# Kernel tuning notes

Hardware: AMD Instinct MI355X
Metric: run time of the kernel (lower is better)

Reference implementation:

```python
import jax, jax.numpy as jnp
import numpy as np

D_MODEL = 1024
N_HEADS = 16
D_K = 64
CHUNK_LEN = 64
B, CHUNKS, NEIGHBORS, NEIGHBOR_LEN = 8, 32, 2, 128
SEQ = CHUNKS * CHUNK_LEN  # 2048
LN_EPS = 1e-5


def setup_inputs() -> dict:
    key = jax.random.key(0)
    ks = jax.random.split(key, 8)
    s = 0.02
    return {
        "h": jax.random.normal(ks[0], (B, SEQ, D_MODEL), dtype=jnp.float32),
        "e": jax.random.normal(ks[1], (B, CHUNKS, NEIGHBORS, NEIGHBOR_LEN, D_MODEL), dtype=jnp.float32),
        "Wq": jax.random.normal(ks[2], (D_MODEL, N_HEADS * D_K), dtype=jnp.float32) * s,
        "bq": jnp.zeros((N_HEADS * D_K,), dtype=jnp.float32),
        "Wk": jax.random.normal(ks[3], (D_MODEL, N_HEADS * D_K), dtype=jnp.float32) * s,
        "bk": jnp.zeros((N_HEADS * D_K,), dtype=jnp.float32),
        "Wv": jax.random.normal(ks[4], (D_MODEL, N_HEADS * D_K), dtype=jnp.float32) * s,
        "bv": jnp.zeros((N_HEADS * D_K,), dtype=jnp.float32),
        "gamma": jnp.ones((D_MODEL,), dtype=jnp.float32),
        "beta": jnp.zeros((D_MODEL,), dtype=jnp.float32),
        "Wo": jax.random.normal(ks[5], (N_HEADS * D_K, D_MODEL), dtype=jnp.float32) * s,
        "bo": jnp.zeros((D_MODEL,), dtype=jnp.float32),
    }


def _layer_norm(x, gamma, beta):
    mu = jnp.mean(x, axis=-1, keepdims=True)
    var = jnp.mean(jnp.square(x - mu), axis=-1, keepdims=True)
    return (x - mu) * jax.lax.rsqrt(var + LN_EPS) * gamma + beta


def reference(h, e, Wq, bq, Wk, bk, Wv, bv, gamma, beta, Wo, bo):
    batch, chunks, neighbors, neighbor_len, d_model = e.shape
    seq = h.shape[1]
    scale = 1.0 / np.sqrt(D_K)
    h_res = h

    # shift so each chunk attends only to completed retrieval chunks
    x = h[:, CHUNK_LEN - 1:]                      # [b, seq-(cl-1), d]
    x = _layer_norm(x, gamma, beta)
    pad = chunks * CHUNK_LEN - x.shape[1]
    x = jnp.pad(x, ((0, 0), (0, pad), (0, 0)))    # [b, chunks*cl, d]
    x = x.reshape(batch, chunks, CHUNK_LEN, d_model)

    q = (x @ Wq + bq).reshape(batch, chunks, CHUNK_LEN, N_HEADS, D_K)
    k = (e @ Wk + bk).reshape(batch, chunks, neighbors, neighbor_len, N_HEADS, D_K)
    v = (e @ Wv + bv).reshape(batch, chunks, neighbors, neighbor_len, N_HEADS, D_K)

    attn = jnp.einsum('bcihd,bcnjhd->bchinj', q, k) * scale   # [b,c,h,i,n,j]
    a_shape = attn.shape
    attn = jax.nn.softmax(attn.reshape(*a_shape[:4], -1), axis=-1).reshape(a_shape)

    o = jnp.einsum('bchinj,bcnjhd->bcihd', attn, v)           # [b,c,i,h,d]
    o = o.reshape(batch, chunks * CHUNK_LEN, N_HEADS * D_K)
    o = o @ Wo + bo
    # undo the shift: left-pad by chunk_len-1, truncate to seq
    o = jnp.pad(o, ((0, 0), (CHUNK_LEN - 1, 0), (0, 0)))[:, :seq]
    return o + h_res
```

## Files before the change

kernel.cpp:

```cpp
#include <hip/hip_runtime.h>
#include <hip/hip_bf16.h>

typedef __attribute__((ext_vector_type(8))) short bf16x8;
typedef __attribute__((ext_vector_type(4))) float f32x4;
typedef __attribute__((ext_vector_type(8))) unsigned short u16x8;

static __device__ __forceinline__ unsigned short f2bf(float f) {
  unsigned int u = __builtin_bit_cast(unsigned int, f);
  u += 0x7fffu + ((u >> 16) & 1u);
  return (unsigned short)(u >> 16);
}
static __device__ __forceinline__ unsigned int pk2(float lo, float hi) {
  return (unsigned int)f2bf(lo) | ((unsigned int)f2bf(hi) << 16);
}
static __device__ __forceinline__ void gload_lds16(const void* g, void* l) {
  __builtin_amdgcn_global_load_lds(
      (__attribute__((address_space(1))) void*)(g),
      (__attribute__((address_space(3))) void*)(l), 16, 0, 0);
}

__global__ __launch_bounds__(256) void cvt_bf16(const float* __restrict__ in,
                                                unsigned short* __restrict__ out,
                                                long n8) {
  const long stride = (long)gridDim.x * 256;
  for (long i = (long)blockIdx.x * 256 + threadIdx.x; i < n8; i += stride) {
    const float4 a = ((const float4*)in)[2 * i];
    const float4 b = ((const float4*)in)[2 * i + 1];
    uint4 w;
    w.x = pk2(a.x, a.y);
    w.y = pk2(a.z, a.w);
    w.z = pk2(b.x, b.y);
    w.w = pk2(b.z, b.w);
    ((uint4*)out)[i] = w;
  }
}

__global__ __launch_bounds__(256) void transpose_all(
    const float* __restrict__ Wq, const float* __restrict__ Wk,
    const float* __restrict__ Wv, const float* __restrict__ Wo,
    unsigned short* __restrict__ wqT, unsigned short* __restrict__ wkvT,
    unsigned short* __restrict__ woT) {
  __shared__ float tile[64][65];
  const int z = blockIdx.z;
  const float* W = (z == 0) ? Wq : (z == 1) ? Wk : (z == 2) ? Wv : Wo;
  unsigned short* WT = (z == 0) ? wqT : (z == 1) ? wkvT : (z == 2) ? (wkvT + 1024 * 1024) : woT;
  const int bx = blockIdx.x;
  const int by = blockIdx.y;
  const int t = threadIdx.x;
  const int rr = t >> 6;
  const int cc = t & 63;
#pragma unroll
  for (int i = 0; i < 16; ++i) {
    int r = i * 4 + rr;
    tile[r][cc] = W[(size_t)(by * 64 + r) * 1024 + bx * 64 + cc];
  }
  __syncthreads();
#pragma unroll
  for (int i = 0; i < 16; ++i) {
    int n = i * 4 + rr;
    WT[(size_t)(bx * 64 + n) * 1024 + by * 64 + cc] = f2bf(tile[cc][n]);
  }
}

__global__ __launch_bounds__(256) void ln_kernel(const float* __restrict__ H,
                                                 const float* __restrict__ gamma,
                                                 const float* __restrict__ beta,
                                                 unsigned short* __restrict__ X) {
  const int row = blockIdx.x;
  const int b = row >> 11;
  const int t = row & 2047;
  const int tid = threadIdx.x;
  uint2* xo = (uint2*)(X + (size_t)row * 1024);
  if (t >= 1985) {
    uint2 z;
    z.x = 0;
    z.y = 0;
    xo[tid] = z;
    return;
  }
  const float4* hp = (const float4*)(H + (size_t)(b * 2048 + t + 63) * 1024);
  float4 v = hp[tid];
  float s = v.x + v.y + v.z + v.w;
  float q = v.x * v.x + v.y * v.y + v.z * v.z + v.w * v.w;
#pragma unroll
  for (int off = 32; off > 0; off >>= 1) {
    s += __shfl_down(s, off);
    q += __shfl_down(q, off);
  }
  __shared__ float red[8];
  const int lane = tid & 63, wid = tid >> 6;
  if (lane == 0) {
    red[wid] = s;
    red[4 + wid] = q;
  }
  __syncthreads();
  s = red[0] + red[1] + red[2] + red[3];
  q = red[4] + red[5] + red[6] + red[7];
  const float mu = s * (1.0f / 1024.0f);
  const float var = q * (1.0f / 1024.0f) - mu * mu;
  const float rs = rsqrtf(var + 1e-5f);
  const float4 g = ((const float4*)gamma)[tid];
  const float4 bb = ((const float4*)beta)[tid];
  uint2 w;
  w.x = pk2((v.x - mu) * rs * g.x + bb.x, (v.y - mu) * rs * g.y + bb.y);
  w.y = pk2((v.z - mu) * rs * g.z + bb.z, (v.w - mu) * rs * g.w + bb.w);
  xo[tid] = w;
}

__global__ __launch_bounds__(256) void fill_head(const float* __restrict__ H,
                                                 float* __restrict__ OUT) {
  const int idx = blockIdx.x * 256 + threadIdx.x;
  const int b = idx / 16128;
  const int rem = idx - b * 16128;
  const size_t off = (size_t)b * 524288 + rem;
  ((float4*)OUT)[off] = ((const float4*)H)[off];
}

#define FENCE_BAR()                                  \
  {                                                  \
    asm volatile("" ::: "memory");                   \
    __builtin_amdgcn_s_barrier();                    \
    __builtin_amdgcn_sched_barrier(0);               \
  }
#define VMW2() asm volatile("s_waitcnt vmcnt(2)" ::: "memory")

#define LDA_(mh, buf)                                                                   \
  {                                                                                     \
    const char* base_ = (const char*)&lds[buf][wm][0];                                  \
    _Pragma("unroll") for (int mi = 0; mi < 4; ++mi) {                                  \
      const int r_ = (mh) * 64 + mi * 16 + lrow;                                        \
      af[mi][0] = *(const bf16x8*)(base_ + r_ * 128 + (((0 + lk) ^ (r_ & 7)) * 16));    \
      af[mi][1] = *(const bf16x8*)(base_ + r_ * 128 + (((4 + lk) ^ (r_ & 7)) * 16));    \
    }                                                                                   \
  }
#define LDB_(nh, buf)                                                                   \
  {                                                                                     \
    const char* base_ = (const char*)&lds[buf][2 + (wn >> 1)][0];                       \
    _Pragma("unroll") for (int ni = 0; ni < 2; ++ni) {                                  \
      const int r_ = (wn & 1) * 64 + (nh) * 32 + ni * 16 + lrow;                        \
      bfr[nh][ni][0] =                                                                  \
          *(const bf16x8*)(base_ + r_ * 128 + (((0 + lk) ^ (r_ & 7)) * 16));            \
      bfr[nh][ni][1] =                                                                  \
          *(const bf16x8*)(base_ + r_ * 128 + (((4 + lk) ^ (r_ & 7)) * 16));            \
    }                                                                                   \
  }
#define MMA_(mh, nh)                                                                    \
  {                                                                                     \
    __builtin_amdgcn_s_setprio(1);                                                      \
    _Pragma("unroll") for (int mi = 0; mi < 4; ++mi)                                    \
        _Pragma("unroll") for (int ni = 0; ni < 2; ++ni) {                              \
      acc[(mh) * 4 + mi][(nh) * 2 + ni] = __builtin_amdgcn_mfma_f32_16x16x32_bf16(      \
          af[mi][0], bfr[nh][ni][0], acc[(mh) * 4 + mi][(nh) * 2 + ni], 0, 0, 0);       \
      acc[(mh) * 4 + mi][(nh) * 2 + ni] = __builtin_amdgcn_mfma_f32_16x16x32_bf16(      \
          af[mi][1], bfr[nh][ni][1], acc[(mh) * 4 + mi][(nh) * 2 + ni], 0, 0, 0);       \
    }                                                                                   \
    __builtin_amdgcn_s_setprio(0);                                                      \
  }

template <int MODE>
__global__ __launch_bounds__(512, 2) void gemm256(
    const unsigned short* __restrict__ A, const unsigned short* __restrict__ BT,
    const float* __restrict__ bias1, const float* __restrict__ bias2,
    unsigned short* __restrict__ C1, unsigned short* __restrict__ C2,
    const float* __restrict__ H, float* __restrict__ OUT) {
  __shared__ alignas(16) unsigned short lds[2][4][128 * 64];
  const int tid = threadIdx.x;
  const int lane = tid & 63;
  const int wid = tid >> 6;
  const int wm = wid >> 2, wn = wid & 3;
  const int lrow = lane & 15, lk = lane >> 4;

  const int nx = gridDim.x;
  const int orig = blockIdx.y * nx + blockIdx.x;
  const int cpx = (nx * gridDim.y) >> 3;
  const int swz = (orig & 7) * cpx + (orig >> 3);
  const int m0 = (swz / nx) * 256;
  const int n0 = (swz % nx) * 256;

  f32x4 acc[8][4] = {};
  bf16x8 af[4][2], bfr[2][2][2];

  auto STAGE = [&](int slot, int kt) {
    const int buf = kt & 1;
    const int kc = kt < 16 ? kt : 15;
    const unsigned short* src = (slot < 2) ? A + (size_t)(m0 + slot * 128) * 1024
                                           : BT + (size_t)(n0 + (slot - 2) * 128) * 1024;
    unsigned short* dst = &lds[buf][slot][0];
#pragma unroll
    for (int l = 0; l < 2; ++l) {
      const int row = l * 64 + wid * 8 + (lane >> 3);
      const int ch = (lane & 7) ^ (row & 7);
      gload_lds16(src + (size_t)row * 1024 + kc * 64 + ch * 8,
                  (char*)dst + (l * 64 + wid * 8) * 128);
    }
  };

  STAGE(0, 0);
  STAGE(1, 0);
  STAGE(2, 0);
  STAGE(3, 0);
  STAGE(0, 1);
  VMW2();
  __builtin_amdgcn_s_barrier();

  for (int it = 0; it < 8; ++it) {
    const int t = 2 * it;
    LDA_(0, 0);
    LDB_(0, 0);
    STAGE(1, t + 1);
    FENCE_BAR();
    MMA_(0, 0);
    FENCE_BAR();
    LDB_(1, 0);
    STAGE(2, t + 1);
    FENCE_BAR();
    MMA_(0, 1);
    FENCE_BAR();
    LDA_(1, 0);
    STAGE(3, t + 1);
    FENCE_BAR();
    MMA_(1, 1);
    FENCE_BAR();
    STAGE(0, t + 2);
    FENCE_BAR();
    MMA_(1, 0);
    VMW2();
    FENCE_BAR();
    LDA_(0, 1);
    LDB_(0, 1);
    STAGE(1, t + 2);
    FENCE_BAR();
    MMA_(0, 0);
    FENCE_BAR();
    LDB_(1, 1);
    STAGE(2, t + 2);
    FENCE_BAR();
    MMA_(0, 1);
    FENCE_BAR();
    LDA_(1, 1);
    STAGE(3, t + 2);
    FENCE_BAR();
    MMA_(1, 1);
    FENCE_BAR();
    STAGE(0, t + 3);
    FENCE_BAR();
    MMA_(1, 0);
    VMW2();
    FENCE_BAR();
  }
  asm volatile("s_waitcnt vmcnt(0)" ::: "memory");
  __syncthreads();

  if (MODE == 0) {
    const float* bsel = (n0 < 1024) ? bias1 : bias2;
    const int cbase = (n0 < 1024) ? n0 : (n0 - 1024);
    unsigned short* Cp0 = (n0 < 1024) ? C1 : C2;
    float bsv[4];
#pragma unroll
    for (int N = 0; N < 4; ++N) bsv[N] = bsel[cbase + wn * 64 + N * 16 + lrow];
    float* arr = (float*)&lds[0][0][0];
    const int q4 = lane >> 4;
#pragma unroll
    for (int p = 0; p < 4; ++p) {
      if (wm == (p >> 1)) {
#pragma unroll
        for (int mb = 0; mb < 4; ++mb) {
          const int M = (p & 1) * 4 + mb;
#pragma unroll
          for (int N = 0; N < 4; ++N) {
            const int cl = wn * 64 + N * 16 + lrow;
#pragma unroll
            for (int r = 0; r < 4; ++r) {
              arr[(mb * 16 + q4 * 4 + r) * 260 + cl] = acc[M][N][r] + bsv[N];
            }
          }
        }
      }
      __syncthreads();
#pragma unroll
      for (int k = 0; k < 4; ++k) {
        const int chunk = k * 512 + tid;
        const int row = chunk >> 5;
        const int c8 = chunk & 31;
        const float* s = arr + row * 260 + c8 * 8;
        float4 f0 = *(const float4*)(s);
        float4 f1 = *(const float4*)(s + 4);
        uint4 w;
        w.x = pk2(f0.x, f0.y);
        w.y = pk2(f0.z, f0.w);
        w.z = pk2(f1.x, f1.y);
        w.w = pk2(f1.z, f1.w);
        *(uint4*)(Cp0 + (size_t)(m0 + p * 64 + row) * 1024 + cbase + c8 * 8) = w;
      }
      __syncthreads();
    }
  } else {
    const int r0 = lane >> 4;
#pragma unroll
    for (int N = 0; N < 4; ++N) {
      const int col = n0 + wn * 64 + N * 16 + lrow;
      const float bsv = bias1[col];
#pragma unroll
      for (int M = 0; M < 8; ++M) {
        const int row = m0 + wm * 128 + M * 16 + r0 * 4;
#pragma unroll
        for (int r = 0; r < 4; ++r) {
          const int gr = row + r;
          if ((gr & 2047) < 1985) {
            const size_t idx = (size_t)(gr + 63) * 1024 + col;
            OUT[idx] = H[idx] + acc[M][N][r] + bsv;
          }
        }
      }
    }
  }
}

__global__ __launch_bounds__(256) void attn_kernel(
    const unsigned short* __restrict__ Q, const unsigned short* __restrict__ K,
    const unsigned short* __restrict__ V, unsigned short* __restrict__ O) {
  __shared__ alignas(16) unsigned short k_lds[256 * 64];
  __shared__ alignas(16) unsigned short v_t[64 * 256];
  const int w = ((blockIdx.x & 7) << 9) | (blockIdx.x >> 3);
  const int h = w & 15;
  const int bc = w >> 4;
  const int tid = threadIdx.x;
  const int lane = tid & 63;
  const int wid = tid >> 6;
  const size_t kv0 = (size_t)bc * 256 * 1024 + h * 64;

  bf16x8 qf[2];
  {
    const size_t qrow = (size_t)bc * 64 + wid * 16 + (lane & 15);
    const unsigned short* qp = Q + qrow * 1024 + h * 64 + (lane >> 4) * 8;
    qf[0] = *(const bf16x8*)(qp);
    qf[1] = *(const bf16x8*)(qp + 32);
  }
#pragma unroll
  for (int it = 0; it < 8; ++it) {
    const int j = it * 32 + (tid >> 3);
    const int c = tid & 7;
    const uint4 kv = *(const uint4*)(K + kv0 + (size_t)j * 1024 + c * 8);
    *(uint4*)((char*)k_lds + j * 128 + ((c ^ (j & 7)) * 16)) = kv;
  }
  {
    const int j = (tid >> 1) * 2;
    const int half = tid & 1;
#pragma unroll
    for (int cc2 = 0; cc2 < 4; ++cc2) {
      const int chunk = half * 4 + cc2;
      const int d0 = chunk * 8;
      u16x8 a = *(const u16x8*)(V + kv0 + (size_t)j * 1024 + d0);
      u16x8 b = *(const u16x8*)(V + kv0 + (size_t)(j + 1) * 1024 + d0);
#pragma unroll
      for (int dd = 0; dd < 8; ++dd) {
        const int d = d0 + dd;
        unsigned int p = (unsigned int)a[dd] | ((unsigned int)b[dd] << 16);
        *(unsigned int*)((char*)v_t + d * 512 + (((j >> 3) ^ (d & 7)) * 16) + ((j & 7) * 2)) = p;
      }
    }
  }
  __syncthreads();

  f32x4 accs[16] = {};
#pragma unroll
  for (int jt = 0; jt < 16; ++jt) {
#pragma unroll
    for (int ks = 0; ks < 2; ++ks) {
      const int r = jt * 16 + (lane & 15);
      bf16x8 kf = *(const bf16x8*)((const char*)k_lds + r * 128 +
                                   (((ks * 4 + (lane >> 4)) ^ (r & 7)) * 16));
      accs[jt] = __builtin_amdgcn_mfma_f32_16x16x32_bf16(qf[ks], kf, accs[jt], 0, 0, 0);
    }
  }
  __syncthreads();

  float inv_[4];
#pragma unroll
  for (int r = 0; r < 4; ++r) {
    float m = accs[0][r];
#pragma unroll
    for (int jt = 1; jt < 16; ++jt) m = fmaxf(m, accs[jt][r]);
#pragma unroll
    for (int mk = 1; mk < 16; mk <<= 1) m = fmaxf(m, __shfl_xor(m, mk));
    float s = 0.f;
#pragma unroll
    for (int jt = 0; jt < 16; ++jt) {
      float p = __expf((accs[jt][r] - m) * 0.125f);
      accs[jt][r] = p;
      s += p;
    }
#pragma unroll
    for (int mk = 1; mk < 16; mk <<= 1) s += __shfl_xor(s, mk);
    inv_[r] = 1.0f / s;
  }
  char* pbase = (char*)k_lds + wid * 8192;
  {
    const int jc = lane & 15;
    const int i0 = (lane >> 4) * 4;
#pragma unroll
    for (int jt = 0; jt < 16; ++jt) {
      const int j = jt * 16 + jc;
#pragma unroll
      for (int r = 0; r < 4; ++r) {
        const int i = i0 + r;
        *(unsigned short*)(pbase + i * 512 + (((j >> 3) ^ (i & 7)) * 16) + ((j & 7) * 2)) =
            f2bf(accs[jt][r] * inv_[r]);
      }
    }
  }
  __syncthreads();

  f32x4 acco[4] = {};
#pragma unroll
  for (int jb = 0; jb < 8; ++jb) {
    const int i = lane & 15;
    bf16x8 pf = *(const bf16x8*)(pbase + i * 512 + (((jb * 4 + (lane >> 4)) ^ (i & 7)) * 16));
#pragma unroll
    for (int ni = 0; ni < 4; ++ni) {
      const int d = ni * 16 + (lane & 15);
      bf16x8 vf = *(const bf16x8*)((const char*)v_t + d * 512 +
                                   (((jb * 4 + (lane >> 4)) ^ (d & 7)) * 16));
      acco[ni] = __builtin_amdgcn_mfma_f32_16x16x32_bf16(pf, vf, acco[ni], 0, 0, 0);
    }
  }
  {
    const size_t row0 = (size_t)bc * 64 + wid * 16 + (lane >> 4) * 4;
#pragma unroll
    for (int ni = 0; ni < 4; ++ni) {
      const int col = h * 64 + ni * 16 + (lane & 15);
#pragma unroll
      for (int r = 0; r < 4; ++r) {
        O[(row0 + r) * 1024 + col] = f2bf(acco[ni][r]);
      }
    }
  }
}

extern "C" void kernel_launch(void* const* d_in, const int* in_sizes, int n_in,
                              void* d_out, int out_size, void* d_ws, size_t ws_size,
                              hipStream_t stream) {
  const float* h = (const float*)d_in[0];
  const float* e = (const float*)d_in[1];
  const float* Wq = (const float*)d_in[2];
  const float* bq = (const float*)d_in[3];
  const float* Wk = (const float*)d_in[4];
  const float* bk = (const float*)d_in[5];
  const float* Wv = (const float*)d_in[6];
  const float* bv = (const float*)d_in[7];
  const float* gamma = (const float*)d_in[8];
  const float* beta = (const float*)d_in[9];
  const float* Wo = (const float*)d_in[10];
  const float* bo = (const float*)d_in[11];
  float* out = (float*)d_out;

  char* ws = (char*)d_ws;
  unsigned short* x = (unsigned short*)ws;
  unsigned short* q = (unsigned short*)(ws + (32ull << 20));
  unsigned short* kbuf = (unsigned short*)(ws + (64ull << 20));
  unsigned short* vbuf = (unsigned short*)(ws + (192ull << 20));
  unsigned short* ebf = (unsigned short*)(ws + (320ull << 20));
  unsigned short* wqT = (unsigned short*)(ws + (448ull << 20));
  unsigned short* wkvT = (unsigned short*)(ws + (450ull << 20));
  unsigned short* woT = (unsigned short*)(ws + (454ull << 20));
  unsigned short* o = x;

  dim3 tb(256);
  cvt_bf16<<<2048, tb, 0, stream>>>(e, ebf, 8388608L);
  transpose_all<<<dim3(16, 16, 4), tb, 0, stream>>>(Wq, Wk, Wv, Wo, wqT, wkvT, woT);
  ln_kernel<<<16384, tb, 0, stream>>>(h, gamma, beta, x);
  gemm256<0><<<dim3(4, 64), dim3(512), 0, stream>>>(x, wqT, bq, nullptr, q, nullptr,
                                                    nullptr, nullptr);
  gemm256<0><<<dim3(8, 256), dim3(512), 0, stream>>>(ebf, wkvT, bk, bv, kbuf, vbuf,
                                                     nullptr, nullptr);
  attn_kernel<<<4096, tb, 0, stream>>>(q, kbuf, vbuf, o);
  fill_head<<<504, tb, 0, stream>>>(h, out);
  gemm256<1><<<dim3(4, 64), dim3(512), 0, stream>>>(o, woT, bo, nullptr, nullptr, nullptr,
                                                    h, out);
}
```

Baseline: 562.7 us.

## Fuse fp32-to-bf16 conversion of e into the K/V projection GEMM

```diff
diff --git a/kernel.cpp b/kernel.cpp
--- a/kernel.cpp
+++ b/kernel.cpp
@@ -17,22 +17,6 @@
   __builtin_amdgcn_global_load_lds(
       (__attribute__((address_space(1))) void*)(g),
       (__attribute__((address_space(3))) void*)(l), 16, 0, 0);
-}
-
-__global__ __launch_bounds__(256) void cvt_bf16(const float* __restrict__ in,
-                                                unsigned short* __restrict__ out,
-                                                long n8) {
-  const long stride = (long)gridDim.x * 256;
-  for (long i = (long)blockIdx.x * 256 + threadIdx.x; i < n8; i += stride) {
-    const float4 a = ((const float4*)in)[2 * i];
-    const float4 b = ((const float4*)in)[2 * i + 1];
-    uint4 w;
-    w.x = pk2(a.x, a.y);
-    w.y = pk2(a.z, a.w);
-    w.z = pk2(b.x, b.y);
-    w.w = pk2(b.z, b.w);
-    ((uint4*)out)[i] = w;
-  }
 }
 
 __global__ __launch_bounds__(256) void transpose_all(
@@ -123,6 +107,8 @@
     __builtin_amdgcn_sched_barrier(0);               \
   }
 #define VMW2() asm volatile("s_waitcnt vmcnt(2)" ::: "memory")
+#define VMW0() asm volatile("s_waitcnt vmcnt(0)" ::: "memory")
+#define LGKM0() asm volatile("s_waitcnt lgkmcnt(0)" ::: "memory")
 
 #define LDA_(mh, buf)                                                                   \
   {                                                                                     \
@@ -131,6 +117,15 @@
       const int r_ = (mh) * 64 + mi * 16 + lrow;                                        \
       af[mi][0] = *(const bf16x8*)(base_ + r_ * 128 + (((0 + lk) ^ (r_ & 7)) * 16));    \
       af[mi][1] = *(const bf16x8*)(base_ + r_ * 128 + (((4 + lk) ^ (r_ & 7)) * 16));    \
+    }                                                                                   \
+  }
+#define LDAX_(mh, buf)                                                                  \
+  {                                                                                     \
+    const char* base_ = (const char*)&lds[buf][wm][0];                                  \
+    _Pragma("unroll") for (int mi = 0; mi < 4; ++mi) {                                  \
+      const int r_ = (mh) * 64 + mi * 16 + lrow;                                        \
+      ax[mi][0] = *(const bf16x8*)(base_ + r_ * 128 + (((0 + lk) ^ (r_ & 7)) * 16));    \
+      ax[mi][1] = *(const bf16x8*)(base_ + r_ * 128 + (((4 + lk) ^ (r_ & 7)) * 16));    \
     }                                                                                   \
   }
 #define LDB_(nh, buf)                                                                   \
@@ -144,22 +139,48 @@
           *(const bf16x8*)(base_ + r_ * 128 + (((4 + lk) ^ (r_ & 7)) * 16));            \
     }                                                                                   \
   }
-#define MMA_(mh, nh)                                                                    \
+#define MMA_(mh, nh, AARR)                                                              \
   {                                                                                     \
     __builtin_amdgcn_s_setprio(1);                                                      \
     _Pragma("unroll") for (int mi = 0; mi < 4; ++mi)                                    \
         _Pragma("unroll") for (int ni = 0; ni < 2; ++ni) {                              \
       acc[(mh) * 4 + mi][(nh) * 2 + ni] = __builtin_amdgcn_mfma_f32_16x16x32_bf16(      \
-          af[mi][0], bfr[nh][ni][0], acc[(mh) * 4 + mi][(nh) * 2 + ni], 0, 0, 0);       \
+          AARR[mi][0], bfr[nh][ni][0], acc[(mh) * 4 + mi][(nh) * 2 + ni], 0, 0, 0);     \
       acc[(mh) * 4 + mi][(nh) * 2 + ni] = __builtin_amdgcn_mfma_f32_16x16x32_bf16(      \
-          af[mi][1], bfr[nh][ni][1], acc[(mh) * 4 + mi][(nh) * 2 + ni], 0, 0, 0);       \
+          AARR[mi][1], bfr[nh][ni][1], acc[(mh) * 4 + mi][(nh) * 2 + ni], 0, 0, 0);     \
     }                                                                                   \
     __builtin_amdgcn_s_setprio(0);                                                      \
   }
-
-template <int MODE>
+#define A_LOADF32(kt)                                                                   \
+  {                                                                                     \
+    const int kc_ = (kt) < 16 ? (kt) : 15;                                              \
+    _Pragma("unroll") for (int s = 0; s < 2; ++s)                                       \
+        _Pragma("unroll") for (int w = 0; w < 2; ++w) {                                 \
+      const float* src_ = Af +                                                          \
+          (size_t)(m0 + s * 128 + wid * 16 + w * 8 + (lane >> 3)) * 1024 +              \
+          kc_ * 64 + (lane & 7) * 8;                                                    \
+      fl[s][w][0] = *(const float4*)src_;                                               \
+      fl[s][w][1] = *(const float4*)(src_ + 4);                                         \
+    }                                                                                   \
+  }
+#define A_WRITE(buf)                                                                    \
+  {                                                                                     \
+    _Pragma("unroll") for (int s = 0; s < 2; ++s)                                       \
+        _Pragma("unroll") for (int w = 0; w < 2; ++w) {                                 \
+      const int r_ = wid * 16 + w * 8 + (lane >> 3);                                    \
+      uint4 wv;                                                                         \
+      wv.x = pk2(fl[s][w][0].x, fl[s][w][0].y);                                         \
+      wv.y = pk2(fl[s][w][0].z, fl[s][w][0].w);                                         \
+      wv.z = pk2(fl[s][w][1].x, fl[s][w][1].y);                                         \
+      wv.w = pk2(fl[s][w][1].z, fl[s][w][1].w);                                         \
+      *(uint4*)((char*)&lds[buf][s][0] + r_ * 128 + ((((lane & 7)) ^ (r_ & 7)) * 16)) = \
+          wv;                                                                           \
+    }                                                                                   \
+  }
+
+template <int MODE, int AF32>
 __global__ __launch_bounds__(512, 2) void gemm256(
-    const unsigned short* __restrict__ A, const unsigned short* __restrict__ BT,
+    const void* __restrict__ Av, const unsigned short* __restrict__ BT,
     const float* __restrict__ bias1, const float* __restrict__ bias2,
     unsigned short* __restrict__ C1, unsigned short* __restrict__ C2,
     const float* __restrict__ H, float* __restrict__ OUT) {
@@ -177,13 +198,17 @@
   const int m0 = (swz / nx) * 256;
   const int n0 = (swz % nx) * 256;
 
+  const unsigned short* Ab = (const unsigned short*)Av;
+  const float* Af = (const float*)Av;
+
   f32x4 acc[8][4] = {};
-  bf16x8 af[4][2], bfr[2][2][2];
+  bf16x8 af[4][2], ax[4][2], bfr[2][2][2];
+  float4 fl[2][2][2];
 
   auto STAGE = [&](int slot, int kt) {
     const int buf = kt & 1;
     const int kc = kt < 16 ? kt : 15;
-    const unsigned short* src = (slot < 2) ? A + (size_t)(m0 + slot * 128) * 1024
+    const unsigned short* src = (slot < 2) ? Ab + (size_t)(m0 + slot * 128) * 1024
                                            : BT + (size_t)(n0 + (slot - 2) * 128) * 1024;
     unsigned short* dst = &lds[buf][slot][0];
 #pragma unroll
@@ -195,60 +220,116 @@
     }
   };
 
-  STAGE(0, 0);
-  STAGE(1, 0);
-  STAGE(2, 0);
-  STAGE(3, 0);
-  STAGE(0, 1);
-  VMW2();
-  __builtin_amdgcn_s_barrier();
-
-  for (int it = 0; it < 8; ++it) {
-    const int t = 2 * it;
-    LDA_(0, 0);
-    LDB_(0, 0);
-    STAGE(1, t + 1);
-    FENCE_BAR();
-    MMA_(0, 0);
-    FENCE_BAR();
-    LDB_(1, 0);
-    STAGE(2, t + 1);
-    FENCE_BAR();
-    MMA_(0, 1);
-    FENCE_BAR();
-    LDA_(1, 0);
-    STAGE(3, t + 1);
-    FENCE_BAR();
-    MMA_(1, 1);
-    FENCE_BAR();
-    STAGE(0, t + 2);
-    FENCE_BAR();
-    MMA_(1, 0);
+  if (AF32 == 0) {
+    STAGE(0, 0);
+    STAGE(1, 0);
+    STAGE(2, 0);
+    STAGE(3, 0);
+    STAGE(0, 1);
     VMW2();
-    FENCE_BAR();
-    LDA_(0, 1);
-    LDB_(0, 1);
-    STAGE(1, t + 2);
-    FENCE_BAR();
-    MMA_(0, 0);
-    FENCE_BAR();
-    LDB_(1, 1);
-    STAGE(2, t + 2);
-    FENCE_BAR();
-    MMA_(0, 1);
-    FENCE_BAR();
-    LDA_(1, 1);
-    STAGE(3, t + 2);
-    FENCE_BAR();
-    MMA_(1, 1);
-    FENCE_BAR();
-    STAGE(0, t + 3);
-    FENCE_BAR();
-    MMA_(1, 0);
-    VMW2();
-    FENCE_BAR();
-  }
-  asm volatile("s_waitcnt vmcnt(0)" ::: "memory");
+    __builtin_amdgcn_s_barrier();
+
+    for (int it = 0; it < 8; ++it) {
+      const int t = 2 * it;
+      LDA_(0, 0);
+      LDB_(0, 0);
+      STAGE(1, t + 1);
+      FENCE_BAR();
+      MMA_(0, 0, af);
+      FENCE_BAR();
+      LDB_(1, 0);
+      STAGE(2, t + 1);
+      FENCE_BAR();
+      MMA_(0, 1, af);
+      FENCE_BAR();
+      LDAX_(1, 0);
+      STAGE(3, t + 1);
+      FENCE_BAR();
+      MMA_(1, 1, ax);
+      FENCE_BAR();
+      STAGE(0, t + 2);
+      FENCE_BAR();
+      MMA_(1, 0, ax);
+      VMW2();
+      FENCE_BAR();
+      LDA_(0, 1);
+      LDB_(0, 1);
+      STAGE(1, t + 2);
+      FENCE_BAR();
+      MMA_(0, 0, af);
+      FENCE_BAR();
+      LDB_(1, 1);
+      STAGE(2, t + 2);
+      FENCE_BAR();
+      MMA_(0, 1, af);
+      FENCE_BAR();
+      LDAX_(1, 1);
+      STAGE(3, t + 2);
+      FENCE_BAR();
+      MMA_(1, 1, ax);
+      FENCE_BAR();
+      STAGE(0, t + 3);
+      FENCE_BAR();
+      MMA_(1, 0, ax);
+      VMW2();
+      FENCE_BAR();
+    }
+  } else {
+    A_LOADF32(0);
+    A_WRITE(0);
+    STAGE(2, 0);
+    STAGE(3, 0);
+    LGKM0();
+    VMW0();
+    __builtin_amdgcn_s_barrier();
+
+    for (int it = 0; it < 8; ++it) {
+      const int t = 2 * it;
+      LDA_(0, 0);
+      LDB_(0, 0);
+      STAGE(2, t + 1);
+      FENCE_BAR();
+      MMA_(0, 0, af);
+      FENCE_BAR();
+      LDB_(1, 0);
+      STAGE(3, t + 1);
+      A_LOADF32(t + 1);
+      FENCE_BAR();
+      MMA_(0, 1, af);
+      FENCE_BAR();
+      LDAX_(1, 0);
+      FENCE_BAR();
+      MMA_(1, 1, ax);
+      FENCE_BAR();
+      A_WRITE(1);
+      MMA_(1, 0, ax);
+      LGKM0();
+      VMW0();
+      FENCE_BAR();
+      LDA_(0, 1);
+      LDB_(0, 1);
+      STAGE(2, t + 2);
+      FENCE_BAR();
+      MMA_(0, 0, af);
+      FENCE_BAR();
+      LDB_(1, 1);
+      STAGE(3, t + 2);
+      A_LOADF32(t + 2);
+      FENCE_BAR();
+      MMA_(0, 1, af);
+      FENCE_BAR();
+      LDAX_(1, 1);
+      FENCE_BAR();
+      MMA_(1, 1, ax);
+      FENCE_BAR();
+      A_WRITE(0);
+      MMA_(1, 0, ax);
+      LGKM0();
+      VMW0();
+      FENCE_BAR();
+    }
+  }
+  VMW0();
   __syncthreads();
 
   if (MODE == 0) {
@@ -459,22 +540,20 @@
   unsigned short* q = (unsigned short*)(ws + (32ull << 20));
   unsigned short* kbuf = (unsigned short*)(ws + (64ull << 20));
   unsigned short* vbuf = (unsigned short*)(ws + (192ull << 20));
-  unsigned short* ebf = (unsigned short*)(ws + (320ull << 20));
   unsigned short* wqT = (unsigned short*)(ws + (448ull << 20));
   unsigned short* wkvT = (unsigned short*)(ws + (450ull << 20));
   unsigned short* woT = (unsigned short*)(ws + (454ull << 20));
   unsigned short* o = x;
 
   dim3 tb(256);
-  cvt_bf16<<<2048, tb, 0, stream>>>(e, ebf, 8388608L);
   transpose_all<<<dim3(16, 16, 4), tb, 0, stream>>>(Wq, Wk, Wv, Wo, wqT, wkvT, woT);
   ln_kernel<<<16384, tb, 0, stream>>>(h, gamma, beta, x);
-  gemm256<0><<<dim3(4, 64), dim3(512), 0, stream>>>(x, wqT, bq, nullptr, q, nullptr,
-                                                    nullptr, nullptr);
-  gemm256<0><<<dim3(8, 256), dim3(512), 0, stream>>>(ebf, wkvT, bk, bv, kbuf, vbuf,
-                                                     nullptr, nullptr);
+  gemm256<0, 0><<<dim3(4, 64), dim3(512), 0, stream>>>(x, wqT, bq, nullptr, q, nullptr,
+                                                       nullptr, nullptr);
+  gemm256<0, 1><<<dim3(8, 256), dim3(512), 0, stream>>>(e, wkvT, bk, bv, kbuf, vbuf,
+                                                        nullptr, nullptr);
   attn_kernel<<<4096, tb, 0, stream>>>(q, kbuf, vbuf, o);
   fill_head<<<504, tb, 0, stream>>>(h, out);
-  gemm256<1><<<dim3(4, 64), dim3(512), 0, stream>>>(o, woT, bo, nullptr, nullptr, nullptr,
-                                                    h, out);
-}
+  gemm256<1, 0><<<dim3(4, 64), dim3(512), 0, stream>>>(o, woT, bo, nullptr, nullptr,
+                                                       nullptr, h, out);
+}
```

After: 846.4 us. 1.5x slower.
